# Kernel tuning notes

Measured on AMD Instinct MI355X. Metric: run time of the kernel, lower is better.

The kernel has to match this reference:

```python
import jax, jax.numpy as jnp
import numpy as np

N_TARGETS = 6
RADIUS = 2
RECLEN = 2 * RADIUS + 1  # 5
SWAP_RC = True


def setup_inputs() -> dict:
    key = jax.random.key(0)
    heatmap = jax.random.uniform(key, (128, 1, 512, 512), dtype=jnp.float32)
    return {"heatmap": heatmap}


def _sample_one(hm):
    # hm: [H, W]. Iteratively: avg-pool (VALID), take first (row-major) argmax
    # of the pooled map, zero the corresponding RECLEN x RECLEN window, repeat.
    H, W = hm.shape
    pw = W - RECLEN + 1  # pooled width

    def step(hm, _):
        # sum-pool == avg-pool up to a positive constant -> same argmax
        agg = jax.lax.reduce_window(
            hm, 0.0, jax.lax.add,
            window_dimensions=(RECLEN, RECLEN),
            window_strides=(1, 1), padding='VALID')
        idx = jnp.argmax(agg)  # first occurrence, row-major (matches torch nonzero()[0])
        r = idx // pw
        c = idx % pw
        # suppress the window in the ORIGINAL heatmap (pooled index i -> window [i, i+RECLEN))
        hm = jax.lax.dynamic_update_slice(
            hm, jnp.zeros((RECLEN, RECLEN), hm.dtype), (r, c))
        return hm, jnp.stack([r + RADIUS, c + RADIUS])

    _, coords = jax.lax.scan(step, hm, None, length=N_TARGETS)
    return coords  # [N_TARGETS, 2] int


def reference(heatmap):
    # heatmap: [B, 1, H, W]
    coords = jax.vmap(_sample_one)(heatmap[:, 0])  # [B, N_TARGETS, 2] as (row, col)
    if SWAP_RC:
        coords = coords[:, :, ::-1]  # (col, row)
    return coords
```

## Files before the change

kernel.cpp:

```cpp
#include <hip/hip_runtime.h>
#include <hip/hip_bf16.h>

#define HM_W 512
#define HM_H 512
#define PW   508

__device__ __forceinline__ void load_row8(const float* __restrict__ hm, int y, int c0, float v[8]) {
    const float4* rp = reinterpret_cast<const float4*>(hm + y * HM_W + c0);
    float4 a = rp[0];
    float4 b = rp[1];
    v[0]=a.x; v[1]=a.y; v[2]=a.z; v[3]=a.w;
    v[4]=b.x; v[5]=b.y; v[6]=b.z; v[7]=b.w;
}

__device__ __forceinline__ void row_best_shfl(const float s[8], int lane, float& bv, int& bc) {
    float cb[12];
#pragma unroll
    for (int j = 0; j < 8; ++j) cb[j] = s[j];
#pragma unroll
    for (int j = 0; j < 4; ++j) cb[8 + j] = __shfl_down(s[j], 1);
    bv = -__builtin_inff();
    bc = 0x7fffffff;
    int c0 = lane * 8;
#pragma unroll
    for (int j = 0; j < 8; ++j) {
        int c = c0 + j;
        float w = cb[j] + cb[j + 1] + cb[j + 2] + cb[j + 3] + cb[j + 4];
        if (c < PW && w > bv) { bv = w; bc = c; }
    }
#pragma unroll
    for (int m = 1; m < 64; m <<= 1) {
        float ov = __shfl_xor(bv, m);
        int   oc = __shfl_xor(bc, m);
        if (ov > bv || (ov == bv && oc < bc)) { bv = ov; bc = oc; }
    }
}

__global__ void phase1_kernel(const float* __restrict__ hm_all,
                              float* __restrict__ rowv_ws, int* __restrict__ rowc_ws) {
    int b = blockIdx.y;
    int wave = threadIdx.x >> 6;
    int lane = threadIdx.x & 63;
    int c0 = lane * 8;
    const float* hm = hm_all + (size_t)b * HM_W * HM_H;

    int rbase = (blockIdx.x * 4 + wave) * 16;
    if (rbase >= PW) return;

    float w0[8], w1[8], w2[8], w3[8], w4[8];
    load_row8(hm, rbase + 0, c0, w0);
    load_row8(hm, rbase + 1, c0, w1);
    load_row8(hm, rbase + 2, c0, w2);
    load_row8(hm, rbase + 3, c0, w3);

#pragma unroll
    for (int rr = 0; rr < 16; ++rr) {
        int y = rbase + rr;
        if (y >= PW) break;
        load_row8(hm, y + 4, c0, w4);
        float s[8];
#pragma unroll
        for (int j = 0; j < 8; ++j)
            s[j] = ((((w0[j] + w1[j]) + w2[j]) + w3[j]) + w4[j]);
        float bv; int bc;
        row_best_shfl(s, lane, bv, bc);
        if (lane == 0) {
            rowv_ws[b * 512 + y] = bv;
            rowc_ws[b * 512 + y] = bc;
        }
#pragma unroll
        for (int j = 0; j < 8; ++j) { w0[j] = w1[j]; w1[j] = w2[j]; w2[j] = w3[j]; w3[j] = w4[j]; }
    }
}

__global__ void __launch_bounds__(640) phase2_kernel(const float* __restrict__ hm_all,
                              const float* __restrict__ rowv_ws,
                              const int* __restrict__ rowc_ws,
                              int* __restrict__ out) {
    int b = blockIdx.x;
    const float* hm = hm_all + (size_t)b * HM_W * HM_H;
    int t = threadIdx.x;
    int wave = t >> 6, lane = t & 63;
    int c0 = lane * 8;

    __shared__ float rowv[512];
    __shared__ int   rowc[512];
    __shared__ float updv[2][9];
    __shared__ int   updc[2][9];
    __shared__ int   upd_y0[2];
    __shared__ int   upd_n[2];

    if (t < 512) {
        if (t < PW) { rowv[t] = rowv_ws[b * 512 + t]; rowc[t] = rowc_ws[b * 512 + t]; }
        else        { rowv[t] = -__builtin_inff();    rowc[t] = 0; }
    }
    if (t == 0) { upd_y0[1] = -1000; upd_n[1] = 0; }

    int zrr[6], zcc[6];

#pragma unroll
    for (int it = 0; it < 6; ++it) {
        __syncthreads();

        int pbuf = (it + 1) & 1;
        int py0 = upd_y0[pbuf];
        int pn  = upd_n[pbuf];

        float bv = -__builtin_inff(); int bi = 0x7fffffff;
#pragma unroll
        for (int j = 0; j < 8; ++j) {
            int idx = j * 64 + lane;
            float v = rowv[idx];
            unsigned u = (unsigned)(idx - py0);
            if (u < (unsigned)pn) v = updv[pbuf][u];
            if (v > bv) { bv = v; bi = idx; }
        }
#pragma unroll
        for (int m = 1; m < 64; m <<= 1) {
            float ov = __shfl_xor(bv, m);
            int   oi = __shfl_xor(bi, m);
            if (ov > bv || (ov == bv && oi < bi)) { bv = ov; bi = oi; }
        }
        int fr = bi;
        unsigned uf = (unsigned)(fr - py0);
        int fc = (uf < (unsigned)pn) ? updc[pbuf][uf] : rowc[fr];
        zrr[it] = fr; zcc[it] = fc;
        if (t == 0) {
            out[b * 12 + it * 2 + 0] = fc + 2;
            out[b * 12 + it * 2 + 1] = fr + 2;
        }

        if (t < 9 && t < pn) {
            int yy = py0 + t;
            rowv[yy] = updv[pbuf][t];
            rowc[yy] = updc[pbuf][t];
        }

        if (it == 5) break;

        int y0 = fr - 4 < 0 ? 0 : fr - 4;
        int y1 = fr + 4 > PW - 1 ? PW - 1 : fr + 4;
        int buf = it & 1;
        int y = y0 + wave;
        if (wave < 9 && y <= y1) {
            float s[8];
#pragma unroll
            for (int j = 0; j < 8; ++j) s[j] = 0.f;
#pragma unroll
            for (int i = 0; i < 5; ++i) {
                float v[8];
                load_row8(hm, y + i, c0, v);
#pragma unroll
                for (int j = 0; j < 8; ++j) {
                    float vv = v[j];
#pragma unroll
                    for (int k = 0; k < 6; ++k) {
                        if (k <= it && (unsigned)(y + i - zrr[k]) < 5u
                                    && (unsigned)(c0 + j - zcc[k]) < 5u)
                            vv = 0.f;
                    }
                    s[j] += vv;
                }
            }
            float nv; int nc;
            row_best_shfl(s, lane, nv, nc);
            if (lane == 0) { updv[buf][wave] = nv; updc[buf][wave] = nc; }
        }
        if (t == 0) { upd_y0[buf] = y0; upd_n[buf] = y1 - y0 + 1; }
    }
}

extern "C" void kernel_launch(void* const* d_in, const int* in_sizes, int n_in,
                              void* d_out, int out_size, void* d_ws, size_t ws_size,
                              hipStream_t stream) {
    const float* hm = (const float*)d_in[0];
    int* out = (int*)d_out;
    float* rowv_ws = (float*)d_ws;
    int*   rowc_ws = (int*)((char*)d_ws + (size_t)128 * 512 * sizeof(float));

    phase1_kernel<<<dim3(8, 128), dim3(256), 0, stream>>>(hm, rowv_ws, rowc_ws);
    phase2_kernel<<<dim3(128), dim3(640), 0, stream>>>(hm, rowv_ws, rowc_ws, out);
}
```

Baseline: 53.30 us.

## Fuse both phases into one kernel with per-batch atomic counters

Merges the row-pooling pass and the iterative suppression pass into a single launch. Phase-2 blocks are appended after the phase-1 blocks and spin on a per-batch atomic counter until all eight producer blocks for that batch have signalled completion. The phase-2 block shrinks from 640 to 256 threads, so each wave now recomputes up to three dirty rows in a loop. This removes the kernel-boundary gap but adds a memset launch and spin-waiting, and it relies on consumer blocks being scheduled after their producers to avoid deadlock.

```diff
diff --git a/kernel.cpp b/kernel.cpp
--- a/kernel.cpp
+++ b/kernel.cpp
@@ -4,6 +4,7 @@
 #define HM_W 512
 #define HM_H 512
 #define PW   508
+#define NBATCH 128
 
 __device__ __forceinline__ void load_row8(const float* __restrict__ hm, int y, int c0, float v[8]) {
     const float4* rp = reinterpret_cast<const float4*>(hm + y * HM_W + c0);
@@ -36,49 +37,9 @@
     }
 }
 
-__global__ void phase1_kernel(const float* __restrict__ hm_all,
-                              float* __restrict__ rowv_ws, int* __restrict__ rowc_ws) {
-    int b = blockIdx.y;
-    int wave = threadIdx.x >> 6;
-    int lane = threadIdx.x & 63;
-    int c0 = lane * 8;
-    const float* hm = hm_all + (size_t)b * HM_W * HM_H;
-
-    int rbase = (blockIdx.x * 4 + wave) * 16;
-    if (rbase >= PW) return;
-
-    float w0[8], w1[8], w2[8], w3[8], w4[8];
-    load_row8(hm, rbase + 0, c0, w0);
-    load_row8(hm, rbase + 1, c0, w1);
-    load_row8(hm, rbase + 2, c0, w2);
-    load_row8(hm, rbase + 3, c0, w3);
-
-#pragma unroll
-    for (int rr = 0; rr < 16; ++rr) {
-        int y = rbase + rr;
-        if (y >= PW) break;
-        load_row8(hm, y + 4, c0, w4);
-        float s[8];
-#pragma unroll
-        for (int j = 0; j < 8; ++j)
-            s[j] = ((((w0[j] + w1[j]) + w2[j]) + w3[j]) + w4[j]);
-        float bv; int bc;
-        row_best_shfl(s, lane, bv, bc);
-        if (lane == 0) {
-            rowv_ws[b * 512 + y] = bv;
-            rowc_ws[b * 512 + y] = bc;
-        }
-#pragma unroll
-        for (int j = 0; j < 8; ++j) { w0[j] = w1[j]; w1[j] = w2[j]; w2[j] = w3[j]; w3[j] = w4[j]; }
-    }
-}
-
-__global__ void __launch_bounds__(640) phase2_kernel(const float* __restrict__ hm_all,
-                              const float* __restrict__ rowv_ws,
-                              const int* __restrict__ rowc_ws,
-                              int* __restrict__ out) {
-    int b = blockIdx.x;
-    const float* hm = hm_all + (size_t)b * HM_W * HM_H;
+__global__ void __launch_bounds__(256) fused_kernel(const float* __restrict__ hm_all,
+                              float* __restrict__ rowv_ws, int* __restrict__ rowc_ws,
+                              int* __restrict__ cnt, int* __restrict__ out) {
     int t = threadIdx.x;
     int wave = t >> 6, lane = t & 63;
     int c0 = lane * 8;
@@ -90,9 +51,55 @@
     __shared__ int   upd_y0[2];
     __shared__ int   upd_n[2];
 
-    if (t < 512) {
-        if (t < PW) { rowv[t] = rowv_ws[b * 512 + t]; rowc[t] = rowc_ws[b * 512 + t]; }
-        else        { rowv[t] = -__builtin_inff();    rowc[t] = 0; }
+    if (blockIdx.x < 1024) {
+        int blk = blockIdx.x;
+        int b = blk >> 3;
+        const float* hm = hm_all + (size_t)b * HM_W * HM_H;
+        int rbase = ((blk & 7) * 4 + wave) * 16;
+
+        float w0[8], w1[8], w2[8], w3[8], w4[8];
+        load_row8(hm, rbase + 0, c0, w0);
+        load_row8(hm, rbase + 1, c0, w1);
+        load_row8(hm, rbase + 2, c0, w2);
+        load_row8(hm, rbase + 3, c0, w3);
+
+#pragma unroll
+        for (int rr = 0; rr < 16; ++rr) {
+            int y = rbase + rr;
+            if (y >= PW) break;
+            load_row8(hm, y + 4, c0, w4);
+            float s[8];
+#pragma unroll
+            for (int j = 0; j < 8; ++j)
+                s[j] = ((((w0[j] + w1[j]) + w2[j]) + w3[j]) + w4[j]);
+            float bv; int bc;
+            row_best_shfl(s, lane, bv, bc);
+            if (lane == 0) {
+                rowv_ws[b * 512 + y] = bv;
+                rowc_ws[b * 512 + y] = bc;
+            }
+#pragma unroll
+            for (int j = 0; j < 8; ++j) { w0[j] = w1[j]; w1[j] = w2[j]; w2[j] = w3[j]; w3[j] = w4[j]; }
+        }
+
+        __syncthreads();
+        if (t == 0)
+            __hip_atomic_fetch_add(&cnt[b], 1, __ATOMIC_RELEASE, __HIP_MEMORY_SCOPE_AGENT);
+        return;
+    }
+
+    int b = blockIdx.x - 1024;
+    const float* hm = hm_all + (size_t)b * HM_W * HM_H;
+
+    if (t == 0) {
+        while (__hip_atomic_load(&cnt[b], __ATOMIC_ACQUIRE, __HIP_MEMORY_SCOPE_AGENT) < 8)
+            __builtin_amdgcn_s_sleep(2);
+    }
+    __syncthreads();
+
+    for (int i = t; i < 512; i += 256) {
+        if (i < PW) { rowv[i] = rowv_ws[b * 512 + i]; rowc[i] = rowc_ws[b * 512 + i]; }
+        else        { rowv[i] = -__builtin_inff();    rowc[i] = 0; }
     }
     if (t == 0) { upd_y0[1] = -1000; upd_n[1] = 0; }
 
@@ -141,30 +148,34 @@
         int y0 = fr - 4 < 0 ? 0 : fr - 4;
         int y1 = fr + 4 > PW - 1 ? PW - 1 : fr + 4;
         int buf = it & 1;
-        int y = y0 + wave;
-        if (wave < 9 && y <= y1) {
-            float s[8];
 #pragma unroll
-            for (int j = 0; j < 8; ++j) s[j] = 0.f;
+        for (int p = 0; p < 3; ++p) {
+            int li = wave + p * 4;
+            int y = y0 + li;
+            if (li < 9 && y <= y1) {
+                float s[8];
 #pragma unroll
-            for (int i = 0; i < 5; ++i) {
-                float v[8];
-                load_row8(hm, y + i, c0, v);
+                for (int j = 0; j < 8; ++j) s[j] = 0.f;
 #pragma unroll
-                for (int j = 0; j < 8; ++j) {
-                    float vv = v[j];
+                for (int i = 0; i < 5; ++i) {
+                    float v[8];
+                    load_row8(hm, y + i, c0, v);
 #pragma unroll
-                    for (int k = 0; k < 6; ++k) {
-                        if (k <= it && (unsigned)(y + i - zrr[k]) < 5u
-                                    && (unsigned)(c0 + j - zcc[k]) < 5u)
-                            vv = 0.f;
+                    for (int j = 0; j < 8; ++j) {
+                        float vv = v[j];
+#pragma unroll
+                        for (int k = 0; k < 6; ++k) {
+                            if (k <= it && (unsigned)(y + i - zrr[k]) < 5u
+                                        && (unsigned)(c0 + j - zcc[k]) < 5u)
+                                vv = 0.f;
+                        }
+                        s[j] += vv;
                     }
-                    s[j] += vv;
                 }
+                float nv; int nc;
+                row_best_shfl(s, lane, nv, nc);
+                if (lane == 0) { updv[buf][li] = nv; updc[buf][li] = nc; }
             }
-            float nv; int nc;
-            row_best_shfl(s, lane, nv, nc);
-            if (lane == 0) { updv[buf][wave] = nv; updc[buf][wave] = nc; }
         }
         if (t == 0) { upd_y0[buf] = y0; upd_n[buf] = y1 - y0 + 1; }
     }
@@ -177,7 +188,8 @@
     int* out = (int*)d_out;
     float* rowv_ws = (float*)d_ws;
     int*   rowc_ws = (int*)((char*)d_ws + (size_t)128 * 512 * sizeof(float));
+    int*   cnt     = (int*)((char*)d_ws + (size_t)2 * 128 * 512 * sizeof(float));
 
-    phase1_kernel<<<dim3(8, 128), dim3(256), 0, stream>>>(hm, rowv_ws, rowc_ws);
-    phase2_kernel<<<dim3(128), dim3(640), 0, stream>>>(hm, rowv_ws, rowc_ws, out);
+    hipMemsetAsync(cnt, 0, NBATCH * sizeof(int), stream);
+    fused_kernel<<<dim3(1024 + NBATCH), dim3(256), 0, stream>>>(hm, rowv_ws, rowc_ws, cnt, out);
 }
```

Result: slower. 103.9 us (+94.9%).
